# Kernel optimization log

Measured on AMD Instinct MI355X. Metric: run time of the kernel, lower is better.

Reference implementation:

```python
import jax, jax.numpy as jnp
import numpy as np

B, N, D = 512, 22, 3
H, TD, AD, L = 128, 32, 32, 4
SIGMA_DATA = 0.168
NORM_CONST = 1.0
E_IN = 2 * H + 1 + 2  # [h_i, h_j, radial, dist_sq, bond_mask]
NUM_ATOM_TYPES = 4
BONDS = [(0, 1), (1, 2), (1, 3), (1, 4), (4, 5), (4, 6), (6, 7), (6, 8), (8, 9), (8, 10),
         (10, 11), (10, 12), (10, 13), (8, 14), (14, 15), (14, 16), (16, 17), (16, 18),
         (18, 19), (18, 20), (18, 21)]
ATOM_TYPES = [0, 1, 0, 0, 1, 2, 3, 0, 1, 0, 1, 0, 0, 0, 1, 2, 3, 0, 1, 0, 0, 0]


def setup_inputs() -> dict:
    key = jax.random.key(0)
    ks = jax.random.split(key, 16)
    xt = jax.random.normal(ks[0], (B, N, D), jnp.float32)
    xt = xt - xt.mean(axis=1, keepdims=True)  # zero center of mass, per assert_mean_zero
    # EDM-style noise levels, strictly positive (log-normal as in compute_loss)
    t = jnp.exp(jax.random.normal(ks[1], (B,), jnp.float32) * 1.2 - 1.2)
    # fully connected edges without self-loops, batched with node offset b*N
    ii, jj = np.meshgrid(np.arange(N), np.arange(N), indexing='ij')
    msk = ii != jj
    ri, ci = ii[msk], jj[msk]  # (N*(N-1),)
    off = (np.arange(B) * N)[:, None]
    row = jnp.asarray((ri[None] + off).reshape(-1), jnp.int32)
    col = jnp.asarray((ci[None] + off).reshape(-1), jnp.int32)
    adj = np.zeros((N, N), np.float32)
    for a, b in BONDS:
        adj[a, b] = 1.0
        adj[b, a] = 1.0
    bond_mask = jnp.asarray(np.tile(adj[ri, ci], B)[:, None], jnp.float32)  # (E,1)
    atom_types = jnp.asarray(ATOM_TYPES, jnp.int32)

    def lin(k, fi, fo):
        return jax.random.normal(k, (fi, fo), jnp.float32) / np.sqrt(fi)

    def per_layer(k, fi, fo):
        return jax.random.normal(k, (L, fi, fo), jnp.float32) / np.sqrt(fi)

    z = lambda *s: jnp.zeros(s, jnp.float32)
    return dict(
        xt=xt, t=t,
        atom_table=jax.random.normal(ks[2], (NUM_ATOM_TYPES, AD), jnp.float32),
        bond_mask=bond_mask,
        W_in=lin(ks[3], TD + AD, H), b_in=z(H),
        ew1=per_layer(ks[4], E_IN, H), eb1=z(L, H),
        ew2=per_layer(ks[5], H, H), eb2=z(L, H),
        aw=per_layer(ks[6], H, 1), ab=z(L, 1),
        cw1=per_layer(ks[7], H, H), cb1=z(L, H),
        cw2=per_layer(ks[8], H, 1) * 0.1,  # coord head, no bias (xavier-small init)
        nw1=per_layer(ks[9], 2 * H, H), nb1=z(L, H),
        nw2=per_layer(ks[10], H, H), nb2=z(L, H),
        row=row, col=col, atom_types=atom_types,
    )


def _sinusoidal(u, dim):
    half = dim // 2
    freqs = jnp.exp(-jnp.log(10000.0) * jnp.arange(half, dtype=jnp.float32) / half)
    a = u[:, None] * freqs
    return jnp.concatenate([jnp.sin(a), jnp.cos(a)], axis=-1)


def reference(xt, t, atom_table, bond_mask, W_in, b_in, ew1, eb1, ew2, eb2,
              aw, ab, cw1, cb1, cw2, nw1, nb1, nw2, nb2, row, col, atom_types):
    BN = B * N
    act = jax.nn.silu
    # EDM preconditioning
    c_in = 1.0 / jnp.sqrt(t ** 2 + SIGMA_DATA ** 2)
    x = (xt * c_in[:, None, None]).reshape(BN, D)
    # node features: time embedding (broadcast per node) + atom-type embedding
    time_emb = jnp.repeat(_sinusoidal(jnp.log(t) / 4.0, TD), N, axis=0)  # (BN,TD)
    atom_emb = jnp.tile(atom_table[atom_types], (B, 1))                  # (BN,AD)
    h = jnp.concatenate([time_emb, atom_emb], axis=1) @ W_in + b_in      # (BN,H)
    # fixed edge attributes: squared distance at input scale + bond mask
    dist_sq0 = jnp.sum((x[row] - x[col]) ** 2, axis=1, keepdims=True)
    edge_attr = jnp.concatenate([dist_sq0, bond_mask], axis=1)           # (E,2)
    for l in range(L):
        diff = x[row] - x[col]                                           # (E,D)
        radial = jnp.sum(diff ** 2, axis=1, keepdims=True)               # (E,1)
        coord_diff = diff / (jnp.sqrt(radial) + NORM_CONST)
        m = jnp.concatenate([h[row], h[col], radial, edge_attr], axis=1)
        m = act(act(m @ ew1[l] + eb1[l]) @ ew2[l] + eb2[l])              # edge MLP (E,H)
        m = m * jax.nn.sigmoid(m @ aw[l] + ab[l])                        # attention gate
        trans = coord_diff * (act(m @ cw1[l] + cb1[l]) @ cw2[l])         # (E,D)
        x = x + jax.ops.segment_sum(trans, row, num_segments=BN)         # agg='sum'
        agg = jax.ops.segment_sum(m, row, num_segments=BN)               # (BN,H)
        h = h + (act(jnp.concatenate([h, agg], axis=1) @ nw1[l] + nb1[l]) @ nw2[l] + nb2[l])
    x_pred = x.reshape(B, N, D)
    x_pred = x_pred - x_pred.mean(axis=1, keepdims=True)                 # remove_mean
    c_skip = SIGMA_DATA ** 2 / (t ** 2 + SIGMA_DATA ** 2)
    c_out = t * SIGMA_DATA / jnp.sqrt(SIGMA_DATA ** 2 + t ** 2)
    return xt * c_skip[:, None, None] + x_pred * c_out[:, None, None]
```

## Files before the change

kernel.cpp:

```cpp
#include <hip/hip_runtime.h>
#include <math.h>

#define NB 512
#define NNODE 22
#define HH 128
#define NEDGE 462
#define NLAYER 4
#define CHUNK2 128
#define NSUP 4
#define SIG 0.168f

#define ASTR 136
#define NSTR 264
#define BSTR 72
#define SLW (128*72)
#define LSLICES 14
#define STAGE_BYTES 36864

typedef __attribute__((ext_vector_type(8))) short short8;
typedef __attribute__((ext_vector_type(4))) short short4v;
typedef __attribute__((ext_vector_type(4))) float f32x4;

#define MFMA_BF16 __builtin_amdgcn_mfma_f32_16x16x32_bf16

__device__ __forceinline__ float siluf(float v) { return v / (1.0f + __expf(-v)); }

__device__ __forceinline__ unsigned short f2bf(float x) {
  union { float f; unsigned u; } v; v.f = x;
  unsigned r = v.u + 0x7FFFu + ((v.u >> 16) & 1u);
  return (unsigned short)(r >> 16);
}
__device__ __forceinline__ float bf2f(unsigned short h) {
  union { unsigned u; float f; } v; v.u = ((unsigned)h) << 16; return v.f;
}
__device__ __forceinline__ void splitbf(float x, unsigned short& hi, unsigned short& lo) {
  union { float f; unsigned u; } v; v.f = x;
  hi = (unsigned short)(v.u >> 16);
  union { unsigned u; float f; } hv; hv.u = ((unsigned)hi) << 16;
  lo = f2bf(x - hv.f);
}

__global__ void prep_weights(const float* __restrict__ ew1, const float* __restrict__ ew2,
                             const float* __restrict__ cw1, const float* __restrict__ nw1,
                             const float* __restrict__ nw2, unsigned short* __restrict__ ws)
{
  int idx = blockIdx.x * 256 + threadIdx.x;
  if (idx >= 4 * LSLICES * 128 * 72) return;
  int kk = idx % 72; int rest = idx / 72;
  int n = rest % 128; rest /= 128;
  int sl = rest % LSLICES; int l = rest / LSLICES;
  float val = 0.f;
  if (kk < 64) {
    if (sl < 4)       val = ew1[((size_t)l * 259 + sl * 64 + kk) * HH + n];
    else if (sl < 6)  val = ew2[((size_t)l * 128 + (sl - 4) * 64 + kk) * HH + n];
    else if (sl < 8)  val = cw1[((size_t)l * 128 + (sl - 6) * 64 + kk) * HH + n];
    else if (sl < 12) val = nw1[((size_t)l * 256 + (sl - 8) * 64 + kk) * HH + n];
    else              val = nw2[((size_t)l * 128 + (sl - 12) * 64 + kk) * HH + n];
  }
  unsigned short hi, lo; splitbf(val, hi, lo);
  size_t base = ((size_t)(l * LSLICES + sl) * 2) * SLW + n * BSTR + kk;
  ws[base]       = hi;
  ws[base + SLW] = lo;
}

__global__ __launch_bounds__(512, 1)
void scorenet_kernel(
    const float* __restrict__ xt, const float* __restrict__ tt,
    const float* __restrict__ atom_table, const float* __restrict__ bond_mask,
    const float* __restrict__ W_in, const float* __restrict__ b_in,
    const float* __restrict__ ew1, const float* __restrict__ eb1,
    const float* __restrict__ eb2,
    const float* __restrict__ aw,  const float* __restrict__ ab,
    const float* __restrict__ cb1, const float* __restrict__ cw2,
    const float* __restrict__ nb1, const float* __restrict__ nb2,
    const int* __restrict__ atom_types,
    const unsigned short* __restrict__ ws,
    float* __restrict__ out)
{
  const int g    = blockIdx.x;
  const int tid  = threadIdx.x;
  const int lane = tid & 63;
  const int wv   = tid >> 6;
  const int ml   = lane & 15;
  const int q    = lane >> 4;
  const int grp  = wv >> 2;
  const int ws4  = wv & 3;
  const int mtn  = wv & 1;
  const int nqn  = wv >> 1;

  __shared__ unsigned short sh_B[2 * SLW];
  __shared__ unsigned short sh_Ah[CHUNK2 * ASTR];
  __shared__ unsigned short sh_Al[CHUNK2 * ASTR];
  __shared__ float sh_Phi[2][NNODE * HH];
  __shared__ float sh_h[NNODE * HH];
  __shared__ float sh_agg[NNODE * HH];
  __shared__ float sh_tail[8 * HH];
  __shared__ float sh_awl[HH], sh_cw2l[HH];
  __shared__ float sh_x[NNODE][3], sh_xacc[NNODE][3];
  __shared__ float sh_d0[NEDGE];
  __shared__ unsigned short sh_bond[NEDGE];
  __shared__ float sh_cd[3][CHUNK2];
  __shared__ float sh_cmul[CHUNK2];
  __shared__ float sh_tf[32], sh_scal[2], sh_mean[3];

  auto issueB = [&](const unsigned short* src) {
    const char* s8 = (const char*)src;
    char* dbase = (char*)&sh_B[0];
    for (int base = wv * 1024; base < STAGE_BYTES; base += 8192) {
      __builtin_amdgcn_global_load_lds(
          (const __attribute__((address_space(1))) unsigned int*)(s8 + base + lane * 16),
          (__attribute__((address_space(3))) unsigned int*)(dbase + base),
          16, 0, 0);
    }
  };

  auto gemmE = [&](f32x4 (&acc)[8], int koff) {
    int arow = (grp * 64 + ws4 * 16 + ml) * ASTR + koff;
#pragma unroll
    for (int sb = 0; sb < 2; sb++) {
      int ak = arow + sb * 32 + q * 8;
      short8 ah = *(const short8*)&sh_Ah[ak];
      short8 al = *(const short8*)&sh_Al[ak];
#pragma unroll
      for (int t = 0; t < 8; t++) {
        int bi = (t * 16 + ml) * BSTR + sb * 32 + q * 8;
        short8 bh = *(const short8*)&sh_B[bi];
        short8 bl = *(const short8*)&sh_B[SLW + bi];
        acc[t] = MFMA_BF16(ah, bh, acc[t], 0, 0, 0);
        acc[t] = MFMA_BF16(ah, bl, acc[t], 0, 0, 0);
        acc[t] = MFMA_BF16(al, bh, acc[t], 0, 0, 0);
      }
    }
  };

  auto gemmN = [&](f32x4 (&acc)[2], int astr, int koff) {
#pragma unroll
    for (int sb = 0; sb < 2; sb++) {
      int ak = (mtn * 16 + ml) * astr + koff + sb * 32 + q * 8;
      short8 ah = *(const short8*)&sh_Ah[ak];
      short8 al = *(const short8*)&sh_Al[ak];
#pragma unroll
      for (int tt = 0; tt < 2; tt++) {
        int bi = ((nqn * 2 + tt) * 16 + ml) * BSTR + sb * 32 + q * 8;
        short8 bh = *(const short8*)&sh_B[bi];
        short8 bl = *(const short8*)&sh_B[SLW + bi];
        acc[tt] = MFMA_BF16(ah, bh, acc[tt], 0, 0, 0);
        acc[tt] = MFMA_BF16(ah, bl, acc[tt], 0, 0, 0);
        acc[tt] = MFMA_BF16(al, bh, acc[tt], 0, 0, 0);
      }
    }
  };

  if (tid == 0) {
    float tg = tt[g];
    sh_scal[0] = rsqrtf(tg * tg + SIG * SIG);
    sh_scal[1] = tg;
  }
  __syncthreads();
  const float c_in = sh_scal[0];
  for (int idx = tid; idx < NNODE * 3; idx += 512) {
    sh_x[idx / 3][idx % 3] = xt[(size_t)g * NNODE * 3 + idx] * c_in;
    sh_xacc[idx / 3][idx % 3] = 0.f;
  }
  if (tid < 32) {
    float u = __logf(sh_scal[1]) * 0.25f;
    int   qq = tid & 15;
    float f = __expf((float)qq * -0.5756462732485115f);
    float a = u * f;
    sh_tf[tid] = (tid < 16) ? __sinf(a) : __cosf(a);
  }
  for (int idx = tid; idx < CHUNK2 * ASTR / 2; idx += 512) {
    ((unsigned*)sh_Ah)[idx] = 0u; ((unsigned*)sh_Al)[idx] = 0u;
  }
  __syncthreads();
  for (int o = tid; o < HH; o += 512) {
    float s = b_in[o];
#pragma unroll 8
    for (int k = 0; k < 32; k++) s += sh_tf[k] * W_in[k * HH + o];
    sh_agg[o] = s;
  }
  for (int idx = tid; idx < 4 * HH; idx += 512) {
    int a = idx >> 7, o = idx & 127;
    float s = 0.f;
#pragma unroll 8
    for (int k = 0; k < 32; k++) s += atom_table[a * 32 + k] * W_in[(32 + k) * HH + o];
    sh_agg[(1 + a) * HH + o] = s;
  }
  for (int e = tid; e < NEDGE; e += 512) {
    int i = e / 21; int r = e - i * 21; int jn = r + (r >= i);
    float dx = sh_x[i][0] - sh_x[jn][0];
    float dy = sh_x[i][1] - sh_x[jn][1];
    float dz = sh_x[i][2] - sh_x[jn][2];
    sh_d0[e]   = dx * dx + dy * dy + dz * dz;
    sh_bond[e] = f2bf(bond_mask[(size_t)g * NEDGE + e]);
  }
  __syncthreads();
  for (int idx = tid; idx < NNODE * HH; idx += 512) {
    int n = idx >> 7, o = idx & 127;
    int at = atom_types[n];
    sh_h[idx] = sh_agg[o] + sh_agg[(1 + at) * HH + o];
  }
  issueB(ws);
  __syncthreads();
  for (int idx = tid; idx < NNODE * HH; idx += 512) sh_agg[idx] = 0.f;

  const f32x4 zf = {0.f, 0.f, 0.f, 0.f};

  for (int l = 0; l < NLAYER; l++) {
    const unsigned short* wsL = ws + (size_t)l * LSLICES * 2 * SLW;
    const float abl = ab[l];

    for (int idx = tid; idx < 8 * HH; idx += 512) {
      int rsel = idx >> 7, n = idx & 127;
      float v;
      switch (rsel) {
        case 0: v = ew1[((size_t)l * 259 + 256) * HH + n]; break;
        case 1: v = ew1[((size_t)l * 259 + 257) * HH + n]; break;
        case 2: v = ew1[((size_t)l * 259 + 258) * HH + n]; break;
        case 3: v = eb1[l * HH + n]; break;
        case 4: v = eb2[l * HH + n]; break;
        case 5: v = cb1[l * HH + n]; break;
        case 6: v = nb1[l * HH + n]; break;
        default: v = nb2[l * HH + n]; break;
      }
      sh_tail[idx] = v;
    }
    if (tid < HH) sh_awl[tid] = aw[l * HH + tid];
    else if (tid < 2 * HH) sh_cw2l[tid - HH] = cw2[l * HH + (tid - HH)];
    for (int idx = tid; idx < NNODE * 16; idx += 512) {
      int nd = idx >> 4, nb = (idx & 15) * 8;
      const float* hp = &sh_h[nd * HH + nb];
      union { short8 v; unsigned short s[8]; } oh, ol;
#pragma unroll
      for (int jj = 0; jj < 8; jj++) { unsigned short hi, lo; splitbf(hp[jj], hi, lo); oh.s[jj] = hi; ol.s[jj] = lo; }
      *(short8*)&sh_Ah[nd * ASTR + nb] = oh.v;
      *(short8*)&sh_Al[nd * ASTR + nb] = ol.v;
    }
    __syncthreads();

    for (int side = 0; side < 2; side++) {
      f32x4 accP[2] = {zf, zf};
      for (int s2 = 0; s2 < 2; s2++) {
        gemmN(accP, ASTR, s2 * 64);
        __syncthreads();
        int st = side * 2 + s2;
        issueB(wsL + (st < 3 ? (st + 1) : 4) * 2 * SLW);
        if (s2 == 0) __syncthreads();
      }
#pragma unroll
      for (int tt = 0; tt < 2; tt++) {
        int col = (nqn * 2 + tt) * 16 + ml;
#pragma unroll
        for (int r = 0; r < 4; r++) {
          int row = mtn * 16 + q * 4 + r;
          if (row < NNODE) sh_Phi[side][row * HH + col] = accP[tt][r];
        }
      }
      __syncthreads();
    }

    for (int sc = 0; sc < NSUP; sc++) {
      const int e0 = sc * CHUNK2;
      {
        int nb = (tid & 15) * 8, eb_ = tid >> 4;
        for (int j4 = 0; j4 < 4; j4++) {
          int el = eb_ + 32 * j4; int e = e0 + el;
          union { short8 v; unsigned short s[8]; } oh, ol;
          if (e < NEDGE) {
            int i = e / 21; int r0 = e - i * 21; int jn = r0 + (r0 >= i);
            float dx = sh_x[i][0] - sh_x[jn][0];
            float dy = sh_x[i][1] - sh_x[jn][1];
            float dz = sh_x[i][2] - sh_x[jn][2];
            float rad = dx * dx + dy * dy + dz * dz;
            float d0v = sh_d0[e], bnd = bf2f(sh_bond[e]);
            const float* pi = &sh_Phi[0][i * HH + nb];
            const float* pj = &sh_Phi[1][jn * HH + nb];
#pragma unroll
            for (int jj = 0; jj < 8; jj++) {
              float v = pi[jj] + pj[jj] +
                        rad * sh_tail[nb + jj] + d0v * sh_tail[128 + nb + jj] +
                        bnd * sh_tail[256 + nb + jj] + sh_tail[384 + nb + jj];
              unsigned short hi, lo; splitbf(siluf(v), hi, lo);
              oh.s[jj] = hi; ol.s[jj] = lo;
            }
          } else {
#pragma unroll
            for (int jj = 0; jj < 8; jj++) { oh.s[jj] = 0; ol.s[jj] = 0; }
          }
          *(short8*)&sh_Ah[el * ASTR + nb] = oh.v;
          *(short8*)&sh_Al[el * ASTR + nb] = ol.v;
        }
      }
      __syncthreads();
      f32x4 acc2[8];
#pragma unroll
      for (int t = 0; t < 8; t++) acc2[t] = zf;
      gemmE(acc2, 0);
      __syncthreads();
      issueB(wsL + 5 * 2 * SLW);
      if (tid < CHUNK2) {
        int e = e0 + tid;
        if (e < NEDGE) {
          int i = e / 21; int r = e - i * 21; int jn = r + (r >= i);
          float dx = sh_x[i][0] - sh_x[jn][0];
          float dy = sh_x[i][1] - sh_x[jn][1];
          float dz = sh_x[i][2] - sh_x[jn][2];
          float inv = 1.0f / (sqrtf(dx * dx + dy * dy + dz * dz) + 1.0f);
          sh_cd[0][tid] = dx * inv; sh_cd[1][tid] = dy * inv; sh_cd[2][tid] = dz * inv;
        } else {
          sh_cd[0][tid] = 0.f; sh_cd[1][tid] = 0.f; sh_cd[2][tid] = 0.f;
        }
      }
      __syncthreads();
      gemmE(acc2, 64);
      __syncthreads();
      issueB(wsL + 6 * 2 * SLW);
      {
        float gpr[4] = {0.f, 0.f, 0.f, 0.f};
#pragma unroll
        for (int t = 0; t < 8; t++) {
          int col = t * 16 + ml;
          float eb2c = sh_tail[512 + col], awc = sh_awl[col];
#pragma unroll
          for (int r = 0; r < 4; r++) {
            float v = siluf(acc2[t][r] + eb2c);
            acc2[t][r] = v;
            gpr[r] += v * awc;
          }
        }
#pragma unroll
        for (int m = 1; m < 16; m <<= 1)
#pragma unroll
          for (int r = 0; r < 4; r++) gpr[r] += __shfl_xor(gpr[r], m, 64);
        float gate[4];
#pragma unroll
        for (int r = 0; r < 4; r++) gate[r] = 1.0f / (1.0f + __expf(-(gpr[r] + abl)));
#pragma unroll
        for (int t = 0; t < 8; t++) {
          int col = t * 16 + ml;
#pragma unroll
          for (int r = 0; r < 4; r++) {
            unsigned short hi, lo; splitbf(acc2[t][r] * gate[r], hi, lo);
            int ai = (grp * 64 + ws4 * 16 + q * 4 + r) * ASTR + col;
            sh_Ah[ai] = hi; sh_Al[ai] = lo;
          }
        }
      }
      __syncthreads();
      f32x4 acc3[8];
#pragma unroll
      for (int t = 0; t < 8; t++) acc3[t] = zf;
      gemmE(acc3, 0);
      __syncthreads();
      issueB(wsL + 7 * 2 * SLW);
      int elast = ((e0 + CHUNK2 < NEDGE) ? e0 + CHUNK2 : NEDGE) - 1;
      int i_lo = e0 / 21, i_hi = elast / 21;
      int nrows = i_hi - i_lo + 1;
      for (int idx = tid; idx < nrows * 32; idx += 512) {
        int i = i_lo + (idx >> 5), fb = (idx & 31) * 4;
        int es = i * 21; if (es < e0) es = e0;
        int ee = i * 21 + 21;
        if (ee > e0 + CHUNK2) ee = e0 + CHUNK2;
        if (ee > NEDGE) ee = NEDGE;
        float* ap = &sh_agg[i * HH + fb];
        float a4[4];
#pragma unroll
        for (int c = 0; c < 4; c++) a4[c] = ap[c];
        for (int e = es; e < ee; e++) {
          union { short4v v; unsigned short s[4]; } uh, ul;
          uh.v = *(const short4v*)&sh_Ah[(e - e0) * ASTR + fb];
          ul.v = *(const short4v*)&sh_Al[(e - e0) * ASTR + fb];
#pragma unroll
          for (int c = 0; c < 4; c++) a4[c] += bf2f(uh.s[c]) + bf2f(ul.s[c]);
        }
#pragma unroll
        for (int c = 0; c < 4; c++) ap[c] = a4[c];
      }
      __syncthreads();
      gemmE(acc3, 64);
      __syncthreads();
      issueB(sc < 3 ? wsL + 4 * 2 * SLW : wsL + 8 * 2 * SLW);
      {
        float cs[4] = {0.f, 0.f, 0.f, 0.f};
#pragma unroll
        for (int t = 0; t < 8; t++) {
          int col = t * 16 + ml;
          float cb1c = sh_tail[640 + col], cwc = sh_cw2l[col];
#pragma unroll
          for (int r = 0; r < 4; r++) cs[r] += siluf(acc3[t][r] + cb1c) * cwc;
        }
#pragma unroll
        for (int m = 1; m < 16; m <<= 1)
#pragma unroll
          for (int r = 0; r < 4; r++) cs[r] += __shfl_xor(cs[r], m, 64);
        if (ml == 0) {
#pragma unroll
          for (int r = 0; r < 4; r++) sh_cmul[grp * 64 + ws4 * 16 + q * 4 + r] = cs[r];
        }
      }
      __syncthreads();
      for (int idx = tid; idx < nrows * 3; idx += 512) {
        int i = i_lo + idx / 3, d = idx % 3;
        int es = i * 21; if (es < e0) es = e0;
        int ee = i * 21 + 21;
        if (ee > e0 + CHUNK2) ee = e0 + CHUNK2;
        if (ee > NEDGE) ee = NEDGE;
        float s = 0.f;
        for (int e = es; e < ee; e++) s += sh_cd[d][e - e0] * sh_cmul[e - e0];
        sh_xacc[i][d] += s;
      }
    }

    for (int idx = tid; idx < NNODE * 32; idx += 512) {
      int nd = idx >> 5, kb = (idx & 31) * 8;
      const float* src = (kb < 128) ? &sh_h[nd * HH + kb] : &sh_agg[nd * HH + (kb - 128)];
      union { short8 v; unsigned short s[8]; } oh, ol;
#pragma unroll
      for (int jj = 0; jj < 8; jj++) { unsigned short hi, lo; splitbf(src[jj], hi, lo); oh.s[jj] = hi; ol.s[jj] = lo; }
      *(short8*)&sh_Ah[nd * NSTR + kb] = oh.v;
      *(short8*)&sh_Al[nd * NSTR + kb] = ol.v;
    }
    __syncthreads();
    {
      f32x4 n1a[2] = {zf, zf};
      for (int s = 0; s < 4; s++) {
        gemmN(n1a, NSTR, s * 64);
        __syncthreads();
        issueB(wsL + (s < 3 ? (9 + s) : 12) * 2 * SLW);
        if (s < 3) __syncthreads();
      }
#pragma unroll
      for (int tt = 0; tt < 2; tt++) {
        int col = (nqn * 2 + tt) * 16 + ml;
        float nb1c = sh_tail[768 + col];
#pragma unroll
        for (int r = 0; r < 4; r++) {
          int row = mtn * 16 + q * 4 + r;
          if (row < NNODE) {
            unsigned short hi, lo; splitbf(siluf(n1a[tt][r] + nb1c), hi, lo);
            sh_Ah[row * ASTR + col] = hi; sh_Al[row * ASTR + col] = lo;
          }
        }
      }
      __syncthreads();
      f32x4 n2a[2] = {zf, zf};
      gemmN(n2a, ASTR, 0);
      __syncthreads();
      issueB(wsL + 13 * 2 * SLW);
      for (int idx = tid; idx < NNODE * 3; idx += 512) {
        int n = idx / 3, d = idx % 3;
        sh_x[n][d] += sh_xacc[n][d];
        sh_xacc[n][d] = 0.f;
      }
      for (int idx = tid; idx < NNODE * HH; idx += 512) sh_agg[idx] = 0.f;
      __syncthreads();
      gemmN(n2a, ASTR, 64);
      __syncthreads();
      if (l < 3) issueB(ws + (size_t)(l + 1) * LSLICES * 2 * SLW);
#pragma unroll
      for (int tt = 0; tt < 2; tt++) {
        int col = (nqn * 2 + tt) * 16 + ml;
        float nb2c = sh_tail[896 + col];
#pragma unroll
        for (int r = 0; r < 4; r++) {
          int row = mtn * 16 + q * 4 + r;
          if (row < NNODE) sh_h[row * HH + col] += n2a[tt][r] + nb2c;
        }
      }
    }
    __syncthreads();
  }

  if (tid < 3) {
    float s = 0.f;
    for (int n = 0; n < NNODE; n++) s += sh_x[n][tid];
    sh_mean[tid] = s * (1.0f / NNODE);
  }
  __syncthreads();
  {
    float tg = sh_scal[1];
    float den = tg * tg + SIG * SIG;
    float c_skip = (SIG * SIG) / den;
    float c_out  = tg * SIG * rsqrtf(den);
    for (int idx = tid; idx < NNODE * 3; idx += 512) {
      int n = idx / 3, d = idx % 3;
      out[(size_t)g * NNODE * 3 + idx] =
          xt[(size_t)g * NNODE * 3 + idx] * c_skip + (sh_x[n][d] - sh_mean[d]) * c_out;
    }
  }
}

extern "C" void kernel_launch(void* const* d_in, const int* in_sizes, int n_in,
                              void* d_out, int out_size, void* d_ws, size_t ws_size,
                              hipStream_t stream) {
  const float* xt         = (const float*)d_in[0];
  const float* t          = (const float*)d_in[1];
  const float* atom_table = (const float*)d_in[2];
  const float* bond_mask  = (const float*)d_in[3];
  const float* W_in       = (const float*)d_in[4];
  const float* b_in       = (const float*)d_in[5];
  const float* ew1        = (const float*)d_in[6];
  const float* eb1        = (const float*)d_in[7];
  const float* ew2        = (const float*)d_in[8];
  const float* eb2        = (const float*)d_in[9];
  const float* aw         = (const float*)d_in[10];
  const float* ab         = (const float*)d_in[11];
  const float* cw1        = (const float*)d_in[12];
  const float* cb1        = (const float*)d_in[13];
  const float* cw2        = (const float*)d_in[14];
  const float* nw1        = (const float*)d_in[15];
  const float* nb1        = (const float*)d_in[16];
  const float* nw2        = (const float*)d_in[17];
  const float* nb2        = (const float*)d_in[18];
  const int* atom_types   = (const int*)d_in[21];

  unsigned short* ws = (unsigned short*)d_ws;

  prep_weights<<<2016, 256, 0, stream>>>(ew1, ew2, cw1, nw1, nw2, ws);

  scorenet_kernel<<<NB, 512, 0, stream>>>(
      xt, t, atom_table, bond_mask, W_in, b_in,
      ew1, eb1, eb2, aw, ab, cb1, cw2, nb1, nb2,
      atom_types, ws, (float*)d_out);
}
```

Baseline: 751.8 us.

## Replace per-node segment loops with register-side LDS atomic scatter

The edge-to-node aggregation of gated messages and coordinate updates now uses LDS atomicAdd straight from the MFMA accumulator registers. This replaces the row-range loops that re-read the bf16 hi/lo split from shared memory, and removes one barrier together with the sh_cmul buffer. Edge endpoint indices are precomputed into byte tables so the divisions by 21 disappear. In exchange there are many shared-memory atomics with contention on the same node rows. Summation order becomes nondeterministic, while aggregation now uses the full fp32 value instead of the hi+lo reconstruction.

Result: slower. 1.299 ms (+72.8%).

```diff
diff --git a/kernel.cpp b/kernel.cpp
--- a/kernel.cpp
+++ b/kernel.cpp
@@ -18,7 +18,6 @@
 #define STAGE_BYTES 36864
 
 typedef __attribute__((ext_vector_type(8))) short short8;
-typedef __attribute__((ext_vector_type(4))) short short4v;
 typedef __attribute__((ext_vector_type(4))) float f32x4;
 
 #define MFMA_BF16 __builtin_amdgcn_mfma_f32_16x16x32_bf16
@@ -99,8 +98,8 @@
   __shared__ float sh_x[NNODE][3], sh_xacc[NNODE][3];
   __shared__ float sh_d0[NEDGE];
   __shared__ unsigned short sh_bond[NEDGE];
+  __shared__ unsigned char sh_ei[NEDGE], sh_ej[NEDGE];
   __shared__ float sh_cd[3][CHUNK2];
-  __shared__ float sh_cmul[CHUNK2];
   __shared__ float sh_tf[32], sh_scal[2], sh_mean[3];
 
   auto issueB = [&](const unsigned short* src) {
@@ -188,6 +187,8 @@
   }
   for (int e = tid; e < NEDGE; e += 512) {
     int i = e / 21; int r = e - i * 21; int jn = r + (r >= i);
+    sh_ei[e] = (unsigned char)i;
+    sh_ej[e] = (unsigned char)jn;
     float dx = sh_x[i][0] - sh_x[jn][0];
     float dy = sh_x[i][1] - sh_x[jn][1];
     float dz = sh_x[i][2] - sh_x[jn][2];
@@ -267,7 +268,7 @@
           int el = eb_ + 32 * j4; int e = e0 + el;
           union { short8 v; unsigned short s[8]; } oh, ol;
           if (e < NEDGE) {
-            int i = e / 21; int r0 = e - i * 21; int jn = r0 + (r0 >= i);
+            int i = sh_ei[e], jn = sh_ej[e];
             float dx = sh_x[i][0] - sh_x[jn][0];
             float dy = sh_x[i][1] - sh_x[jn][1];
             float dz = sh_x[i][2] - sh_x[jn][2];
@@ -301,7 +302,7 @@
       if (tid < CHUNK2) {
         int e = e0 + tid;
         if (e < NEDGE) {
-          int i = e / 21; int r = e - i * 21; int jn = r + (r >= i);
+          int i = sh_ei[e], jn = sh_ej[e];
           float dx = sh_x[i][0] - sh_x[jn][0];
           float dy = sh_x[i][1] - sh_x[jn][1];
           float dz = sh_x[i][2] - sh_x[jn][2];
@@ -340,7 +341,9 @@
           int col = t * 16 + ml;
 #pragma unroll
           for (int r = 0; r < 4; r++) {
-            unsigned short hi, lo; splitbf(acc2[t][r] * gate[r], hi, lo);
+            float vg = acc2[t][r] * gate[r];
+            acc2[t][r] = vg;
+            unsigned short hi, lo; splitbf(vg, hi, lo);
             int ai = (grp * 64 + ws4 * 16 + q * 4 + r) * ASTR + col;
             sh_Ah[ai] = hi; sh_Al[ai] = lo;
           }
@@ -353,28 +356,21 @@
       gemmE(acc3, 0);
       __syncthreads();
       issueB(wsL + 7 * 2 * SLW);
-      int elast = ((e0 + CHUNK2 < NEDGE) ? e0 + CHUNK2 : NEDGE) - 1;
-      int i_lo = e0 / 21, i_hi = elast / 21;
-      int nrows = i_hi - i_lo + 1;
-      for (int idx = tid; idx < nrows * 32; idx += 512) {
-        int i = i_lo + (idx >> 5), fb = (idx & 31) * 4;
-        int es = i * 21; if (es < e0) es = e0;
-        int ee = i * 21 + 21;
-        if (ee > e0 + CHUNK2) ee = e0 + CHUNK2;
-        if (ee > NEDGE) ee = NEDGE;
-        float* ap = &sh_agg[i * HH + fb];
-        float a4[4];
-#pragma unroll
-        for (int c = 0; c < 4; c++) a4[c] = ap[c];
-        for (int e = es; e < ee; e++) {
-          union { short4v v; unsigned short s[4]; } uh, ul;
-          uh.v = *(const short4v*)&sh_Ah[(e - e0) * ASTR + fb];
-          ul.v = *(const short4v*)&sh_Al[(e - e0) * ASTR + fb];
-#pragma unroll
-          for (int c = 0; c < 4; c++) a4[c] += bf2f(uh.s[c]) + bf2f(ul.s[c]);
-        }
-#pragma unroll
-        for (int c = 0; c < 4; c++) ap[c] = a4[c];
+      {
+        int nodes[4]; bool emask[4];
+#pragma unroll
+        for (int r = 0; r < 4; r++) {
+          int e = e0 + grp * 64 + ws4 * 16 + q * 4 + r;
+          emask[r] = (e < NEDGE);
+          nodes[r] = emask[r] ? (int)sh_ei[e] : 0;
+        }
+#pragma unroll
+        for (int t = 0; t < 8; t++) {
+          int col = t * 16 + ml;
+#pragma unroll
+          for (int r = 0; r < 4; r++)
+            if (emask[r]) atomicAdd(&sh_agg[nodes[r] * HH + col], acc2[t][r]);
+        }
       }
       __syncthreads();
       gemmE(acc3, 64);
@@ -393,21 +389,15 @@
         for (int m = 1; m < 16; m <<= 1)
 #pragma unroll
           for (int r = 0; r < 4; r++) cs[r] += __shfl_xor(cs[r], m, 64);
-        if (ml == 0) {
-#pragma unroll
-          for (int r = 0; r < 4; r++) sh_cmul[grp * 64 + ws4 * 16 + q * 4 + r] = cs[r];
-        }
-      }
-      __syncthreads();
-      for (int idx = tid; idx < nrows * 3; idx += 512) {
-        int i = i_lo + idx / 3, d = idx % 3;
-        int es = i * 21; if (es < e0) es = e0;
-        int ee = i * 21 + 21;
-        if (ee > e0 + CHUNK2) ee = e0 + CHUNK2;
-        if (ee > NEDGE) ee = NEDGE;
-        float s = 0.f;
-        for (int e = es; e < ee; e++) s += sh_cd[d][e - e0] * sh_cmul[e - e0];
-        sh_xacc[i][d] += s;
+        if (ml < 3) {
+#pragma unroll
+          for (int r = 0; r < 4; r++) {
+            int le = grp * 64 + ws4 * 16 + q * 4 + r;
+            int e = e0 + le;
+            if (e < NEDGE)
+              atomicAdd(&sh_xacc[sh_ei[e]][ml], sh_cd[ml][le] * cs[r]);
+          }
+        }
       }
     }
 
```

## Retile edge GEMMs to 32x64 per wave and defer attention gate scaling

Applied to the files above, without the earlier changes.

Each of the 8 waves now computes a 32-row by 64-column tile instead of 16 rows by 128 columns. Each B fragment loaded from LDS is therefore reused across two A row tiles, which cuts shared-memory B traffic per MFMA. Because a row's gate reduction now spans two waves, the ungated SiLU output is written to LDS and the sigmoid gate is applied afterwards, both inside the third GEMM's activation and in the aggregation. This relies on the gate being a per-row scalar, so it commutes with the matmul. The change also caches edge i/j indices and bond flags in byte arrays instead of recomputing divisions, and truncates the low bf16 split instead of rounding it, which slightly changes precision.

After: 703.0 us. 1.07x faster.

```diff
diff --git a/kernel.cpp b/kernel.cpp
--- a/kernel.cpp
+++ b/kernel.cpp
@@ -37,7 +37,8 @@
   union { float f; unsigned u; } v; v.f = x;
   hi = (unsigned short)(v.u >> 16);
   union { unsigned u; float f; } hv; hv.u = ((unsigned)hi) << 16;
-  lo = f2bf(x - hv.f);
+  union { float f; unsigned u; } w; w.f = x - hv.f;
+  lo = (unsigned short)(w.u >> 16);
 }
 
 __global__ void prep_weights(const float* __restrict__ ew1, const float* __restrict__ ew2,
@@ -57,7 +58,11 @@
     else if (sl < 12) val = nw1[((size_t)l * 256 + (sl - 8) * 64 + kk) * HH + n];
     else              val = nw2[((size_t)l * 128 + (sl - 12) * 64 + kk) * HH + n];
   }
-  unsigned short hi, lo; splitbf(val, hi, lo);
+  unsigned short hi, lo;
+  { union { float f; unsigned u; } v; v.f = val;
+    hi = (unsigned short)(v.u >> 16);
+    union { unsigned u; float f; } hv; hv.u = ((unsigned)hi) << 16;
+    lo = f2bf(val - hv.f); }
   size_t base = ((size_t)(l * LSLICES + sl) * 2) * SLW + n * BSTR + kk;
   ws[base]       = hi;
   ws[base + SLW] = lo;
@@ -83,14 +88,14 @@
   const int wv   = tid >> 6;
   const int ml   = lane & 15;
   const int q    = lane >> 4;
-  const int grp  = wv >> 2;
-  const int ws4  = wv & 3;
+  const int mp   = wv >> 1;
+  const int nh2  = wv & 1;
   const int mtn  = wv & 1;
   const int nqn  = wv >> 1;
 
-  __shared__ unsigned short sh_B[2 * SLW];
-  __shared__ unsigned short sh_Ah[CHUNK2 * ASTR];
-  __shared__ unsigned short sh_Al[CHUNK2 * ASTR];
+  __shared__ __align__(16) unsigned short sh_B[2 * SLW];
+  __shared__ __align__(16) unsigned short sh_Ah[CHUNK2 * ASTR];
+  __shared__ __align__(16) unsigned short sh_Al[CHUNK2 * ASTR];
   __shared__ float sh_Phi[2][NNODE * HH];
   __shared__ float sh_h[NNODE * HH];
   __shared__ float sh_agg[NNODE * HH];
@@ -98,9 +103,11 @@
   __shared__ float sh_awl[HH], sh_cw2l[HH];
   __shared__ float sh_x[NNODE][3], sh_xacc[NNODE][3];
   __shared__ float sh_d0[NEDGE];
-  __shared__ unsigned short sh_bond[NEDGE];
+  __shared__ unsigned char sh_ei[NEDGE];
+  __shared__ unsigned char sh_ej[NEDGE];
   __shared__ float sh_cd[3][CHUNK2];
-  __shared__ float sh_cmul[CHUNK2];
+  __shared__ float sh_red[CHUNK2][2];
+  __shared__ float sh_gate[CHUNK2];
   __shared__ float sh_tf[32], sh_scal[2], sh_mean[3];
 
   auto issueB = [&](const unsigned short* src) {
@@ -114,21 +121,27 @@
     }
   };
 
-  auto gemmE = [&](f32x4 (&acc)[8], int koff) {
-    int arow = (grp * 64 + ws4 * 16 + ml) * ASTR + koff;
+  auto gemmE = [&](f32x4 (&acc)[2][4], int koff) {
+    int arow0 = (mp * 32 + ml) * ASTR + koff;
+    int arow1 = arow0 + 16 * ASTR;
 #pragma unroll
     for (int sb = 0; sb < 2; sb++) {
-      int ak = arow + sb * 32 + q * 8;
-      short8 ah = *(const short8*)&sh_Ah[ak];
-      short8 al = *(const short8*)&sh_Al[ak];
-#pragma unroll
-      for (int t = 0; t < 8; t++) {
-        int bi = (t * 16 + ml) * BSTR + sb * 32 + q * 8;
+      int k8 = sb * 32 + q * 8;
+      short8 ah0 = *(const short8*)&sh_Ah[arow0 + k8];
+      short8 al0 = *(const short8*)&sh_Al[arow0 + k8];
+      short8 ah1 = *(const short8*)&sh_Ah[arow1 + k8];
+      short8 al1 = *(const short8*)&sh_Al[arow1 + k8];
+#pragma unroll
+      for (int t = 0; t < 4; t++) {
+        int bi = ((nh2 * 4 + t) * 16 + ml) * BSTR + k8;
         short8 bh = *(const short8*)&sh_B[bi];
         short8 bl = *(const short8*)&sh_B[SLW + bi];
-        acc[t] = MFMA_BF16(ah, bh, acc[t], 0, 0, 0);
-        acc[t] = MFMA_BF16(ah, bl, acc[t], 0, 0, 0);
-        acc[t] = MFMA_BF16(al, bh, acc[t], 0, 0, 0);
+        acc[0][t] = MFMA_BF16(ah0, bh, acc[0][t], 0, 0, 0);
+        acc[0][t] = MFMA_BF16(ah0, bl, acc[0][t], 0, 0, 0);
+        acc[0][t] = MFMA_BF16(al0, bh, acc[0][t], 0, 0, 0);
+        acc[1][t] = MFMA_BF16(ah1, bh, acc[1][t], 0, 0, 0);
+        acc[1][t] = MFMA_BF16(ah1, bl, acc[1][t], 0, 0, 0);
+        acc[1][t] = MFMA_BF16(al1, bh, acc[1][t], 0, 0, 0);
       }
     }
   };
@@ -188,11 +201,13 @@
   }
   for (int e = tid; e < NEDGE; e += 512) {
     int i = e / 21; int r = e - i * 21; int jn = r + (r >= i);
+    float bm = bond_mask[(size_t)g * NEDGE + e];
+    sh_ei[e] = (unsigned char)(i | ((bm != 0.f) ? 0x80 : 0));
+    sh_ej[e] = (unsigned char)jn;
     float dx = sh_x[i][0] - sh_x[jn][0];
     float dy = sh_x[i][1] - sh_x[jn][1];
     float dz = sh_x[i][2] - sh_x[jn][2];
-    sh_d0[e]   = dx * dx + dy * dy + dz * dz;
-    sh_bond[e] = f2bf(bond_mask[(size_t)g * NEDGE + e]);
+    sh_d0[e] = dx * dx + dy * dy + dz * dz;
   }
   __syncthreads();
   for (int idx = tid; idx < NNODE * HH; idx += 512) {
@@ -267,12 +282,13 @@
           int el = eb_ + 32 * j4; int e = e0 + el;
           union { short8 v; unsigned short s[8]; } oh, ol;
           if (e < NEDGE) {
-            int i = e / 21; int r0 = e - i * 21; int jn = r0 + (r0 >= i);
+            int c = sh_ei[e]; int i = c & 31; int jn = sh_ej[e];
+            float bnd = (float)(c >> 7);
             float dx = sh_x[i][0] - sh_x[jn][0];
             float dy = sh_x[i][1] - sh_x[jn][1];
             float dz = sh_x[i][2] - sh_x[jn][2];
             float rad = dx * dx + dy * dy + dz * dz;
-            float d0v = sh_d0[e], bnd = bf2f(sh_bond[e]);
+            float d0v = sh_d0[e];
             const float* pi = &sh_Phi[0][i * HH + nb];
             const float* pj = &sh_Phi[1][jn * HH + nb];
 #pragma unroll
@@ -292,16 +308,18 @@
         }
       }
       __syncthreads();
-      f32x4 acc2[8];
-#pragma unroll
-      for (int t = 0; t < 8; t++) acc2[t] = zf;
+      f32x4 acc2[2][4];
+#pragma unroll
+      for (int m2i = 0; m2i < 2; m2i++)
+#pragma unroll
+        for (int t = 0; t < 4; t++) acc2[m2i][t] = zf;
       gemmE(acc2, 0);
       __syncthreads();
       issueB(wsL + 5 * 2 * SLW);
       if (tid < CHUNK2) {
         int e = e0 + tid;
         if (e < NEDGE) {
-          int i = e / 21; int r = e - i * 21; int jn = r + (r >= i);
+          int i = sh_ei[e] & 31, jn = sh_ej[e];
           float dx = sh_x[i][0] - sh_x[jn][0];
           float dy = sh_x[i][1] - sh_x[jn][1];
           float dz = sh_x[i][2] - sh_x[jn][2];
@@ -316,40 +334,49 @@
       __syncthreads();
       issueB(wsL + 6 * 2 * SLW);
       {
-        float gpr[4] = {0.f, 0.f, 0.f, 0.f};
-#pragma unroll
-        for (int t = 0; t < 8; t++) {
-          int col = t * 16 + ml;
-          float eb2c = sh_tail[512 + col], awc = sh_awl[col];
-#pragma unroll
-          for (int r = 0; r < 4; r++) {
-            float v = siluf(acc2[t][r] + eb2c);
-            acc2[t][r] = v;
-            gpr[r] += v * awc;
+        float gpr[2][4];
+#pragma unroll
+        for (int m2i = 0; m2i < 2; m2i++)
+#pragma unroll
+          for (int r = 0; r < 4; r++) gpr[m2i][r] = 0.f;
+#pragma unroll
+        for (int m2i = 0; m2i < 2; m2i++) {
+#pragma unroll
+          for (int t = 0; t < 4; t++) {
+            int col = nh2 * 64 + t * 16 + ml;
+            float eb2c = sh_tail[512 + col], awc = sh_awl[col];
+#pragma unroll
+            for (int r = 0; r < 4; r++) {
+              float v = siluf(acc2[m2i][t][r] + eb2c);
+              gpr[m2i][r] += v * awc;
+              unsigned short hi, lo; splitbf(v, hi, lo);
+              int ai = (mp * 32 + m2i * 16 + q * 4 + r) * ASTR + col;
+              sh_Ah[ai] = hi; sh_Al[ai] = lo;
+            }
           }
         }
 #pragma unroll
         for (int m = 1; m < 16; m <<= 1)
 #pragma unroll
-          for (int r = 0; r < 4; r++) gpr[r] += __shfl_xor(gpr[r], m, 64);
-        float gate[4];
-#pragma unroll
-        for (int r = 0; r < 4; r++) gate[r] = 1.0f / (1.0f + __expf(-(gpr[r] + abl)));
-#pragma unroll
-        for (int t = 0; t < 8; t++) {
-          int col = t * 16 + ml;
-#pragma unroll
-          for (int r = 0; r < 4; r++) {
-            unsigned short hi, lo; splitbf(acc2[t][r] * gate[r], hi, lo);
-            int ai = (grp * 64 + ws4 * 16 + q * 4 + r) * ASTR + col;
-            sh_Ah[ai] = hi; sh_Al[ai] = lo;
-          }
-        }
-      }
-      __syncthreads();
-      f32x4 acc3[8];
-#pragma unroll
-      for (int t = 0; t < 8; t++) acc3[t] = zf;
+          for (int m2i = 0; m2i < 2; m2i++)
+#pragma unroll
+            for (int r = 0; r < 4; r++) gpr[m2i][r] += __shfl_xor(gpr[m2i][r], m, 64);
+        if (ml == 0) {
+#pragma unroll
+          for (int m2i = 0; m2i < 2; m2i++)
+#pragma unroll
+            for (int r = 0; r < 4; r++)
+              sh_red[mp * 32 + m2i * 16 + q * 4 + r][nh2] = gpr[m2i][r];
+        }
+      }
+      __syncthreads();
+      if (tid < CHUNK2)
+        sh_gate[tid] = 1.0f / (1.0f + __expf(-(sh_red[tid][0] + sh_red[tid][1] + abl)));
+      f32x4 acc3[2][4];
+#pragma unroll
+      for (int m2i = 0; m2i < 2; m2i++)
+#pragma unroll
+        for (int t = 0; t < 4; t++) acc3[m2i][t] = zf;
       gemmE(acc3, 0);
       __syncthreads();
       issueB(wsL + 7 * 2 * SLW);
@@ -367,11 +394,12 @@
 #pragma unroll
         for (int c = 0; c < 4; c++) a4[c] = ap[c];
         for (int e = es; e < ee; e++) {
+          float gg = sh_gate[e - e0];
           union { short4v v; unsigned short s[4]; } uh, ul;
           uh.v = *(const short4v*)&sh_Ah[(e - e0) * ASTR + fb];
           ul.v = *(const short4v*)&sh_Al[(e - e0) * ASTR + fb];
 #pragma unroll
-          for (int c = 0; c < 4; c++) a4[c] += bf2f(uh.s[c]) + bf2f(ul.s[c]);
+          for (int c = 0; c < 4; c++) a4[c] += gg * (bf2f(uh.s[c]) + bf2f(ul.s[c]));
         }
 #pragma unroll
         for (int c = 0; c < 4; c++) ap[c] = a4[c];
@@ -381,21 +409,36 @@
       __syncthreads();
       issueB(sc < 3 ? wsL + 4 * 2 * SLW : wsL + 8 * 2 * SLW);
       {
-        float cs[4] = {0.f, 0.f, 0.f, 0.f};
-#pragma unroll
-        for (int t = 0; t < 8; t++) {
-          int col = t * 16 + ml;
-          float cb1c = sh_tail[640 + col], cwc = sh_cw2l[col];
-#pragma unroll
-          for (int r = 0; r < 4; r++) cs[r] += siluf(acc3[t][r] + cb1c) * cwc;
+        float cs[2][4];
+#pragma unroll
+        for (int m2i = 0; m2i < 2; m2i++) {
+          float g4[4];
+#pragma unroll
+          for (int r = 0; r < 4; r++) {
+            g4[r] = sh_gate[mp * 32 + m2i * 16 + q * 4 + r];
+            cs[m2i][r] = 0.f;
+          }
+#pragma unroll
+          for (int t = 0; t < 4; t++) {
+            int col = nh2 * 64 + t * 16 + ml;
+            float cb1c = sh_tail[640 + col], cwc = sh_cw2l[col];
+#pragma unroll
+            for (int r = 0; r < 4; r++)
+              cs[m2i][r] += siluf(g4[r] * acc3[m2i][t][r] + cb1c) * cwc;
+          }
         }
 #pragma unroll
         for (int m = 1; m < 16; m <<= 1)
 #pragma unroll
-          for (int r = 0; r < 4; r++) cs[r] += __shfl_xor(cs[r], m, 64);
+          for (int m2i = 0; m2i < 2; m2i++)
+#pragma unroll
+            for (int r = 0; r < 4; r++) cs[m2i][r] += __shfl_xor(cs[m2i][r], m, 64);
         if (ml == 0) {
 #pragma unroll
-          for (int r = 0; r < 4; r++) sh_cmul[grp * 64 + ws4 * 16 + q * 4 + r] = cs[r];
+          for (int m2i = 0; m2i < 2; m2i++)
+#pragma unroll
+            for (int r = 0; r < 4; r++)
+              sh_red[mp * 32 + m2i * 16 + q * 4 + r][nh2] = cs[m2i][r];
         }
       }
       __syncthreads();
@@ -406,7 +449,8 @@
         if (ee > e0 + CHUNK2) ee = e0 + CHUNK2;
         if (ee > NEDGE) ee = NEDGE;
         float s = 0.f;
-        for (int e = es; e < ee; e++) s += sh_cd[d][e - e0] * sh_cmul[e - e0];
+        for (int e = es; e < ee; e++)
+          s += sh_cd[d][e - e0] * (sh_red[e - e0][0] + sh_red[e - e0][1]);
         sh_xacc[i][d] += s;
       }
     }
```
